# Performance work log

Hardware: AMD Instinct MI355X
Metric: run time of the kernel (lower is better)

Reference implementation:

```python
import jax, jax.numpy as jnp
import numpy as np

B, C, M, T = 2, 512, 16, 128
H = 8
D = C // H  # 64, divisible by 4 for 2D RoPE
G = C // 4  # GroupNorm groups = 128
S = M * T


def group_norm(x, scale, bias, groups=G, eps=1e-5):
    b, c, m, t = x.shape
    xg = x.reshape(b, groups, c // groups, m, t)
    mu = xg.mean(axis=(2, 3, 4), keepdims=True)
    var = xg.var(axis=(2, 3, 4), keepdims=True)
    xn = ((xg - mu) * jax.lax.rsqrt(var + eps)).reshape(b, c, m, t)
    return xn * scale[None, :, None, None] + bias[None, :, None, None]


def dwsep_conv(x, dw, pw):
    # depthwise 3x3 (groups=C) then pointwise 1x1
    y = jax.lax.conv_general_dilated(
        x, dw, window_strides=(1, 1), padding='SAME',
        dimension_numbers=('NCHW', 'HWIO', 'NCHW'), feature_group_count=x.shape[1])
    return jnp.einsum('bcmt,cd->bdmt', y, pw)


def rope2d(x):
    # x: [B,H,M,T,D]; first D/2 dims rotated by freq index m, last D/2 by time index t
    d = x.shape[-1]
    dh = d // 2
    q = dh // 2
    inv = 1.0 / (10000.0 ** (jnp.arange(q, dtype=jnp.float32) / q))

    def rot(v, ang):
        h = v.shape[-1] // 2
        v1, v2 = v[..., :h], v[..., h:]
        c, s = jnp.cos(ang), jnp.sin(ang)
        return jnp.concatenate([v1 * c - v2 * s, v1 * s + v2 * c], axis=-1)

    ang_f = jnp.arange(x.shape[2], dtype=jnp.float32)[:, None] * inv  # [M,q]
    ang_t = jnp.arange(x.shape[3], dtype=jnp.float32)[:, None] * inv  # [T,q]
    xf = rot(x[..., :dh], ang_f[:, None, :])  # broadcast over T
    xt = rot(x[..., dh:], ang_t)
    return jnp.concatenate([xf, xt], axis=-1)


def setup_inputs() -> dict:
    key = jax.random.key(0)
    ks = jax.random.split(key, 14)
    s = 0.02
    return {
        'x': jax.random.normal(ks[0], (B, C, M, T), jnp.float32),
        'lengths': jax.random.randint(ks[1], (B,), T // 2, T + 1),
        'gn_scale': jnp.ones((C,), jnp.float32),
        'gn_bias': jnp.zeros((C,), jnp.float32),
        'dw_q': jax.random.normal(ks[2], (3, 3, 1, C), jnp.float32) * s,
        'dw_k': jax.random.normal(ks[3], (3, 3, 1, C), jnp.float32) * s,
        'dw_v': jax.random.normal(ks[4], (3, 3, 1, C), jnp.float32) * s,
        'pw_q': jax.random.normal(ks[5], (C, C), jnp.float32) * s,
        'pw_k': jax.random.normal(ks[6], (C, C), jnp.float32) * s,
        'pw_v': jax.random.normal(ks[7], (C, C), jnp.float32) * s,
        'attn_w': jax.random.normal(ks[8], (C, C), jnp.float32) * s,
        'attn_b': jnp.zeros((C,), jnp.float32),
        'out_w': jax.random.normal(ks[9], (C, C), jnp.float32) * s,
        'out_b': jnp.zeros((C,), jnp.float32),
    }


def reference(x, lengths, gn_scale, gn_bias, dw_q, dw_k, dw_v, pw_q, pw_k, pw_v,
              attn_w, attn_b, out_w, out_b):
    residual = x
    xn = group_norm(x, gn_scale, gn_bias)

    def to_heads(y):  # [B,C,M,T] -> [B,H,M,T,D]
        return y.reshape(B, H, D, M, T).transpose(0, 1, 3, 4, 2)

    q = rope2d(to_heads(dwsep_conv(xn, dw_q, pw_q)))
    k = rope2d(to_heads(dwsep_conv(xn, dw_k, pw_k)))
    v = to_heads(dwsep_conv(xn, dw_v, pw_v))

    q = q.reshape(B, H, S, D)
    k = k.reshape(B, H, S, D)
    v = v.reshape(B, H, S, D)

    scores = jnp.einsum('bhsd,bhkd->bhsk', q, k) / np.sqrt(D).astype(np.float32)
    valid_t = jnp.arange(T)[None, :] < lengths[:, None]        # [B,T]
    valid = jnp.tile(valid_t, (1, M))                          # [B,S], token idx = m*T + t
    scores = jnp.where(valid[:, None, None, :], scores, jnp.float32(-1e9))
    attn = jax.nn.softmax(scores, axis=-1)
    o = jnp.einsum('bhsk,bhkd->bhsd', attn, v)                 # [B,H,S,D]

    o = o.transpose(0, 2, 1, 3).reshape(B, S, C)
    o = o @ attn_w + attn_b                                    # block output proj
    o = o.reshape(B, M, T, C).transpose(0, 3, 1, 2)            # [B,C,M,T]
    out = jnp.einsum('bcmt,cd->bdmt', o, out_w) + out_b[None, :, None, None]
    return residual + out
```

## Files before the change

kernel.cpp:

```cpp
#include <hip/hip_runtime.h>
#include <math.h>

#define CCH 512
#define SSQ 2048
#define MTOT 4096

typedef __bf16 bf16;
typedef __bf16 bf16x8 __attribute__((ext_vector_type(8)));
typedef __bf16 bf16x4 __attribute__((ext_vector_type(4)));
typedef float  f32x4  __attribute__((ext_vector_type(4)));

#define AS1 __attribute__((address_space(1)))
#define AS3 __attribute__((address_space(3)))
__device__ __forceinline__ void glds16(const void* g, void* l) {
    __builtin_amdgcn_global_load_lds((const AS1 void*)g, (AS3 void*)l, 16, 0, 0);
}

__global__ __launch_bounds__(256) void gnw_kernel(const float* __restrict__ x,
        float* __restrict__ mu, float* __restrict__ rstd,
        const float* __restrict__ w0, const float* __restrict__ w1,
        const float* __restrict__ w2, const float* __restrict__ w3,
        const float* __restrict__ w4, bf16* __restrict__ wT) {
    __shared__ float smem[64*65];
    int tid = threadIdx.x;
    if (blockIdx.x < 256) {
        float* s_sum = smem;
        float* s_sq  = smem + 256;
        int bg = blockIdx.x;
        long base = (long)bg * 8192;
        float sum = 0.f, sq = 0.f;
#pragma unroll
        for (int r = 0; r < 32; ++r) {
            float v = x[base + r*256 + tid];
            sum += v; sq += v*v;
        }
        s_sum[tid] = sum; s_sq[tid] = sq;
        __syncthreads();
        for (int off = 128; off > 0; off >>= 1) {
            if (tid < off) { s_sum[tid] += s_sum[tid+off]; s_sq[tid] += s_sq[tid+off]; }
            __syncthreads();
        }
        if (tid == 0) {
            float m = s_sum[0] * (1.f/8192.f);
            float v = s_sq[0]  * (1.f/8192.f) - m*m;
            mu[bg] = m;
            rstd[bg] = rsqrtf(v + 1e-5f);
        }
    } else {
        int bid = blockIdx.x - 256;
        int z = bid >> 6, r2 = bid & 63;
        int k0 = (r2 >> 3)*64, n0 = (r2 & 7)*64;
        const float* srcs[5] = {w0, w1, w2, w3, w4};
        const float* W = srcs[z];
        bf16* D = wT + (long)z * (CCH*CCH);
        float (*t)[65] = (float(*)[65])smem;
        int cI = tid & 63, r4 = tid >> 6;
#pragma unroll
        for (int p = 0; p < 16; ++p) {
            int kr = p*4 + r4;
            t[kr][cI] = W[(long)(k0+kr)*CCH + n0 + cI];
        }
        __syncthreads();
#pragma unroll
        for (int p = 0; p < 16; ++p) {
            int nr = p*4 + r4;
            D[(long)(n0+nr)*CCH + k0 + cI] = (bf16)t[cI][nr];
        }
    }
}

__global__ void tn_kernel(const float* __restrict__ x, const float* __restrict__ mu,
                          const float* __restrict__ rstd, const float* __restrict__ gsc,
                          const float* __restrict__ gbs, bf16* __restrict__ xnT) {
    __shared__ float t[64][65];
    int s0 = blockIdx.x*64, c0 = blockIdx.y*64, b = blockIdx.z;
    int tid = threadIdx.x;
    int cI = tid & 63, r4 = tid >> 6;
#pragma unroll
    for (int p = 0; p < 16; ++p) {
        int cr = p*4 + r4;
        t[cr][cI] = x[((long)(b*CCH + c0 + cr))*SSQ + s0 + cI];
    }
    __syncthreads();
#pragma unroll
    for (int p = 0; p < 16; ++p) {
        int sr = p*4 + r4;
        int c = c0 + cI;
        int g = b*128 + (c >> 2);
        float v = (t[cI][sr] - mu[g]) * rstd[g] * gsc[c] + gbs[c];
        xnT[((long)(b*SSQ + s0 + sr))*CCH + c] = (bf16)v;
    }
}

__global__ __launch_bounds__(256) void dw3_kernel(const bf16* __restrict__ xnT,
        const float* __restrict__ dwq, const float* __restrict__ dwk,
        const float* __restrict__ dwv,
        bf16* __restrict__ yq, bf16* __restrict__ yk, bf16* __restrict__ yv) {
    int tid = threadIdx.x;
    int cc = (tid & 63) * 8;
    int s  = blockIdx.x*4 + (tid >> 6);
    int sl = s & (SSQ-1);
    int b  = s >> 11;
    int m = sl >> 7, t = sl & 127;
    float aq[8] = {}, ak[8] = {}, av[8] = {};
#pragma unroll
    for (int di = 0; di < 3; ++di) {
        int m2 = m + di - 1;
        if ((unsigned)m2 >= 16u) continue;
#pragma unroll
        for (int dj = 0; dj < 3; ++dj) {
            int t2 = t + dj - 1;
            if ((unsigned)t2 >= 128u) continue;
            bf16x8 xv = *(const bf16x8*)(xnT + ((long)(b*SSQ + m2*128 + t2))*CCH + cc);
            int wi = (di*3 + dj)*CCH + cc;
#pragma unroll
            for (int i = 0; i < 8; ++i) {
                float xf = (float)xv[i];
                aq[i] += xf * dwq[wi+i];
                ak[i] += xf * dwk[wi+i];
                av[i] += xf * dwv[wi+i];
            }
        }
    }
    bf16x8 oq, ok, ov;
#pragma unroll
    for (int i = 0; i < 8; ++i) { oq[i] = (bf16)aq[i]; ok[i] = (bf16)ak[i]; ov[i] = (bf16)av[i]; }
    long o = (long)s*CCH + cc;
    *(bf16x8*)(yq + o) = oq;
    *(bf16x8*)(yk + o) = ok;
    *(bf16x8*)(yv + o) = ov;
}

template<int NFR>
__device__ __forceinline__ void gemm_core128(const bf16* __restrict__ A,
        const bf16* __restrict__ Wt, int m0, int n0,
        bf16* As, bf16* Bs, f32x4 (&acc)[4][NFR]) {
    int tid = threadIdx.x, lane = tid & 63, wid = tid >> 6;
    int sw = wid & 1, nw = wid >> 1;
    int col = lane & 15, quad = lane >> 4;
    const char* gA[4]; char* ldsA[4];
#pragma unroll
    for (int p = 0; p < 4; ++p) {
        int ci = tid + p*256;
        int row = ci >> 3;
        int c = (ci & 7) ^ (row & 7);
        gA[p] = (const char*)A + ((long)(m0+row)*CCH + c*8)*2;
        ldsA[p] = (char*)As + ci*16;
    }
    const char* gB[NFR]; char* ldsB[NFR];
#pragma unroll
    for (int p = 0; p < NFR; ++p) {
        int ci = tid + p*256;
        int row = ci >> 3;
        int c = (ci & 7) ^ (row & 7);
        gB[p] = (const char*)Wt + ((long)(n0+row)*CCH + c*8)*2;
        ldsB[p] = (char*)Bs + ci*16;
    }
    int rowA = sw*64 + col;
    int rowB = nw*(NFR*16) + col;
    for (int k0 = 0; k0 < CCH; k0 += 64) {
        __syncthreads();
#pragma unroll
        for (int p = 0; p < 4; ++p)   glds16(gA[p] + k0*2, ldsA[p]);
#pragma unroll
        for (int p = 0; p < NFR; ++p) glds16(gB[p] + k0*2, ldsB[p]);
        __syncthreads();
        bf16x8 af[4][2], bfr[NFR][2];
#pragma unroll
        for (int mt = 0; mt < 4; ++mt) {
            int r = rowA + mt*16;
#pragma unroll
            for (int ks = 0; ks < 2; ++ks) {
                int c = (ks*4 + quad) ^ (r & 7);
                af[mt][ks] = *(const bf16x8*)((char*)As + r*128 + c*16);
            }
        }
#pragma unroll
        for (int nt = 0; nt < NFR; ++nt) {
            int r = rowB + nt*16;
#pragma unroll
            for (int ks = 0; ks < 2; ++ks) {
                int c = (ks*4 + quad) ^ (r & 7);
                bfr[nt][ks] = *(const bf16x8*)((char*)Bs + r*128 + c*16);
            }
        }
#pragma unroll
        for (int ks = 0; ks < 2; ++ks)
#pragma unroll
            for (int mt = 0; mt < 4; ++mt)
#pragma unroll
                for (int nt = 0; nt < NFR; ++nt)
                    acc[mt][nt] = __builtin_amdgcn_mfma_f32_16x16x32_bf16(
                        af[mt][ks], bfr[nt][ks], acc[mt][nt], 0,0,0);
    }
}

__global__ __launch_bounds__(256) void gemm_qkv(const bf16* __restrict__ Abase,
        const bf16* __restrict__ wT, bf16* __restrict__ qout,
        bf16* __restrict__ kout, bf16* __restrict__ vout) {
    __shared__ bf16 As[128*64];
    __shared__ bf16 Bs[64*64];
    int m0 = blockIdx.x*128, n0 = blockIdx.y*64, z = blockIdx.z;
    f32x4 acc[4][2] = {};
    gemm_core128<2>(Abase + (long)z*MTOT*CCH, wT + (long)z*CCH*CCH, m0, n0, As, Bs, acc);
    int tid = threadIdx.x, lane = tid & 63, wid = tid >> 6;
    int sw = wid & 1, nw = wid >> 1;
    int col = lane & 15, quad = lane >> 4;
    int nb = n0 + nw*32, mb = m0 + sw*64;
    if (z < 2) {
        bf16* outp = z ? kout : qout;
        const float sc = z ? 1.0f : 0.125f;
        float invf = __expf(-(float)col * 0.5756462732485114f);
        bool tHalf = (nb & 32) != 0;
#pragma unroll
        for (int mt = 0; mt < 4; ++mt)
#pragma unroll
            for (int r = 0; r < 4; ++r) {
                int row = mb + mt*16 + quad*4 + r;
                int sl = row & (SSQ-1);
                float pos = tHalf ? (float)(sl & 127) : (float)(sl >> 7);
                float ang = pos * invf;
                float sn, cs;
                __sincosf(ang, &sn, &cs);
                float x1 = acc[mt][0][r], x2 = acc[mt][1][r];
                outp[(long)row*CCH + nb + col]      = (bf16)((x1*cs - x2*sn)*sc);
                outp[(long)row*CCH + nb + 16 + col] = (bf16)((x1*sn + x2*cs)*sc);
            }
    } else {
#pragma unroll
        for (int mt = 0; mt < 4; ++mt)
#pragma unroll
            for (int nt = 0; nt < 2; ++nt) {
                int n = nb + nt*16 + col;
                int row0 = mb + mt*16 + quad*4;
                int bq = row0 >> 11, sl0 = row0 & (SSQ-1);
                bf16x4 pk;
#pragma unroll
                for (int r = 0; r < 4; ++r) pk[r] = (bf16)acc[mt][nt][r];
                *(bf16x4*)(vout + ((long)(bq*CCH + n))*SSQ + sl0) = pk;
            }
    }
}

template<int MODE>
__global__ __launch_bounds__(256) void gemm_bf16(const bf16* __restrict__ A,
        const bf16* __restrict__ Wt, const float* __restrict__ bias,
        const float* __restrict__ resid, void* __restrict__ outv) {
    __shared__ bf16 As[128*64];
    __shared__ bf16 Bs[64*64];
    int m0 = blockIdx.x*128, n0 = blockIdx.y*64;
    f32x4 acc[4][2] = {};
    gemm_core128<2>(A, Wt, m0, n0, As, Bs, acc);
    int tid = threadIdx.x, lane = tid & 63, wid = tid >> 6;
    int sw = wid & 1, nw = wid >> 1;
    int col = lane & 15, quad = lane >> 4;
    int nb = n0 + nw*32, mb = m0 + sw*64;
    if (MODE == 3) {
        bf16* outp = (bf16*)outv;
#pragma unroll
        for (int nt = 0; nt < 2; ++nt) {
            int n = nb + nt*16 + col;
            float bv = bias[n];
#pragma unroll
            for (int mt = 0; mt < 4; ++mt)
#pragma unroll
                for (int r = 0; r < 4; ++r)
                    outp[(long)(mb + mt*16 + quad*4 + r)*CCH + n] = (bf16)(acc[mt][nt][r] + bv);
        }
    } else {
        float* outp = (float*)outv;
#pragma unroll
        for (int mt = 0; mt < 4; ++mt)
#pragma unroll
            for (int nt = 0; nt < 2; ++nt) {
                int n = nb + nt*16 + col;
                float bv = bias[n];
                int row0 = mb + mt*16 + quad*4;
                int b = row0 >> 11, sl0 = row0 & (SSQ-1);
                long off = ((long)(b*CCH + n))*SSQ + sl0;
                float4 rr = *(const float4*)(resid + off);
                float4 o4;
                o4.x = acc[mt][nt][0] + bv + rr.x;
                o4.y = acc[mt][nt][1] + bv + rr.y;
                o4.z = acc[mt][nt][2] + bv + rr.z;
                o4.w = acc[mt][nt][3] + bv + rr.w;
                *(float4*)(outp + off) = o4;
            }
    }
}

__global__ __launch_bounds__(256) void attn_kernel(
        const bf16* __restrict__ qb, const bf16* __restrict__ kb,
        const bf16* __restrict__ vb, const int* __restrict__ lengths,
        float* __restrict__ opart, float* __restrict__ lpart) {
    __shared__ char KV[2][16384];
    __shared__ bf16 Ps[4][32*72];
    int bid = blockIdx.x;
    int bh = bid & 15;
    int n  = bid >> 4;
    int qt = n & 15, kvh = n >> 4;
    int b = bh >> 3, h = bh & 7;
    int tid = threadIdx.x, wid = tid >> 6, lane = tid & 63;
    int col = lane & 15, quad = lane >> 4;
    int lenb = lengths[b];
    int q0 = qt*128 + wid*32;
    int k0 = kvh*1024;

    const char* gp[4]; long gstep[4]; int ldsoff[4];
#pragma unroll
    for (int p = 0; p < 4; ++p) {
        int idx = tid + p*256;
        int isV = idx >> 9;
        int rem = idx & 511;
        int r = rem >> 3;
        int csrc = (rem & 7) ^ (r & 7);
        if (!isV) { gp[p] = (const char*)kb + ((long)(b*SSQ + k0 + r))*1024 + h*128 + csrc*16; gstep[p] = 65536; }
        else      { gp[p] = (const char*)vb + ((long)(b*CCH + h*64 + r))*4096 + (long)k0*2 + csrc*16; gstep[p] = 128; }
        ldsoff[p] = idx*16;
    }

    f32x4 mb[4];
#pragma unroll
    for (int sub = 0; sub < 4; ++sub)
#pragma unroll
        for (int r = 0; r < 4; ++r)
            mb[sub][r] = (64 + sub*16 + quad*4 + r < lenb) ? 0.f : -10000.f;

    const bf16* qp = qb + (long)(b*SSQ)*CCH + h*64;
    bf16x8 qf[2][2];
#pragma unroll
    for (int qt2 = 0; qt2 < 2; ++qt2)
#pragma unroll
        for (int dc = 0; dc < 2; ++dc)
            qf[qt2][dc] = *(const bf16x8*)(qp + (long)(q0 + qt2*16 + col)*CCH + dc*32 + quad*8);

    f32x4 of[2][4] = {};
    float ls0 = 0.f, ls1 = 0.f;
    bf16* pw = Ps[wid];
    int cswz = col & 7;

#pragma unroll
    for (int p = 0; p < 4; ++p) glds16(gp[p], KV[0] + ldsoff[p]);
    __syncthreads();

    for (int t = 0; t < 16; ++t) {
        if (t < 15) {
#pragma unroll
            for (int p = 0; p < 4; ++p)
                glds16(gp[p] + (long)(t+1)*gstep[p], KV[(t+1) & 1] + ldsoff[p]);
        }
        const bf16* K = (const bf16*)(KV[t & 1]);
        const bf16* V = (const bf16*)(KV[t & 1] + 8192);
        bool masked = ((kvh*16 + t) & 1) != 0;
        f32x4 sc[4][2];
#pragma unroll
        for (int sub = 0; sub < 4; ++sub)
#pragma unroll
            for (int qt2 = 0; qt2 < 2; ++qt2)
                sc[sub][qt2] = masked ? mb[sub] : (f32x4){0.f,0.f,0.f,0.f};
#pragma unroll
        for (int sub = 0; sub < 4; ++sub)
#pragma unroll
            for (int dc = 0; dc < 2; ++dc) {
                bf16x8 kf = *(const bf16x8*)((const char*)K + (sub*16 + col)*128 + (((dc*4+quad) ^ cswz))*16);
#pragma unroll
                for (int qt2 = 0; qt2 < 2; ++qt2)
                    sc[sub][qt2] = __builtin_amdgcn_mfma_f32_16x16x32_bf16(
                        kf, qf[qt2][dc], sc[sub][qt2], 0,0,0);
            }
#pragma unroll
        for (int sub = 0; sub < 4; ++sub)
#pragma unroll
            for (int qt2 = 0; qt2 < 2; ++qt2) {
                bf16x4 pk;
#pragma unroll
                for (int r = 0; r < 4; ++r) {
                    float p = __expf(sc[sub][qt2][r]);
                    if (qt2) ls1 += p; else ls0 += p;
                    pk[r] = (bf16)p;
                }
                *(bf16x4*)(pw + (qt2*16 + col)*72 + sub*16 + quad*4) = pk;
            }
#pragma unroll
        for (int ks = 0; ks < 2; ++ks) {
            bf16x8 pf0 = *(const bf16x8*)(pw + col*72 + ks*32 + quad*8);
            bf16x8 pf1 = *(const bf16x8*)(pw + (16 + col)*72 + ks*32 + quad*8);
#pragma unroll
            for (int dt = 0; dt < 4; ++dt) {
                bf16x8 vf = *(const bf16x8*)((const char*)V + (dt*16 + col)*128 + (((ks*4+quad) ^ cswz))*16);
                of[0][dt] = __builtin_amdgcn_mfma_f32_16x16x32_bf16(pf0, vf, of[0][dt], 0,0,0);
                of[1][dt] = __builtin_amdgcn_mfma_f32_16x16x32_bf16(pf1, vf, of[1][dt], 0,0,0);
            }
        }
        __syncthreads();
    }

    ls0 += __shfl_xor(ls0, 16); ls0 += __shfl_xor(ls0, 32);
    ls1 += __shfl_xor(ls1, 16); ls1 += __shfl_xor(ls1, 32);

    float* op = opart + ((long)(kvh*16 + bh)*2048)*64;
#pragma unroll
    for (int qt2 = 0; qt2 < 2; ++qt2)
#pragma unroll
        for (int dt = 0; dt < 4; ++dt)
#pragma unroll
            for (int r = 0; r < 4; ++r)
                op[(long)(q0 + qt2*16 + quad*4 + r)*64 + dt*16 + col] = of[qt2][dt][r];
    if (quad == 0) {
        float* lp = lpart + (long)(kvh*16 + bh)*2048;
        lp[q0 + col]      = ls0;
        lp[q0 + 16 + col] = ls1;
    }
}

__global__ __launch_bounds__(256) void attn_merge(const float* __restrict__ opart,
        const float* __restrict__ lpart, bf16* __restrict__ o) {
    int idx = blockIdx.x*256 + threadIdx.x;
    int dchunk = idx & 15;
    int q = (idx >> 4) & 2047;
    int bh = idx >> 15;
    long o0 = ((long)bh*2048 + q)*64 + dchunk*4;
    float4 a = *(const float4*)(opart + o0);
    float4 c = *(const float4*)(opart + o0 + (long)16*2048*64);
    float inv = 1.f / (lpart[bh*2048 + q] + lpart[(16 + bh)*2048 + q]);
    bf16x4 pk;
    pk[0] = (bf16)((a.x + c.x) * inv);
    pk[1] = (bf16)((a.y + c.y) * inv);
    pk[2] = (bf16)((a.z + c.z) * inv);
    pk[3] = (bf16)((a.w + c.w) * inv);
    int b = bh >> 3, h = bh & 7;
    *(bf16x4*)(o + ((long)(b*SSQ + q))*CCH + h*64 + dchunk*4) = pk;
}

extern "C" void kernel_launch(void* const* d_in, const int* in_sizes, int n_in,
                              void* d_out, int out_size, void* d_ws, size_t ws_size,
                              hipStream_t stream) {
    const float* x        = (const float*)d_in[0];
    const int*   lengths  = (const int*)  d_in[1];
    const float* gn_scale = (const float*)d_in[2];
    const float* gn_bias  = (const float*)d_in[3];
    const float* dw_q     = (const float*)d_in[4];
    const float* dw_k     = (const float*)d_in[5];
    const float* dw_v     = (const float*)d_in[6];
    const float* pw_q     = (const float*)d_in[7];
    const float* pw_k     = (const float*)d_in[8];
    const float* pw_v     = (const float*)d_in[9];
    const float* attn_w   = (const float*)d_in[10];
    const float* attn_b   = (const float*)d_in[11];
    const float* out_w    = (const float*)d_in[12];
    const float* out_b    = (const float*)d_in[13];
    float* out = (float*)d_out;

    char* w = (char*)d_ws;
    float* mu   = (float*)w;
    float* rstd = (float*)(w + 1024);
    bf16* wT    = (bf16*)(w + 4096);
    bf16* wTa = wT + 3*CCH*CCH;
    bf16* wTo = wT + 4*CCH*CCH;
    float* lpart = (float*)(w + 0x00290000);
    bf16* xnT  = (bf16*)(w + 0x00300000);
    bf16* yT   = (bf16*)(w + 0x00700000);
    float* opart = (float*)(w + 0x00300000);
    bf16* qbf  = (bf16*)(w + 0x01300000);
    bf16* kbf  = (bf16*)(w + 0x01700000);
    bf16* vbf  = (bf16*)(w + 0x01B00000);
    bf16* obf  = (bf16*)(w + 0x01F00000);
    bf16* tmpb = (bf16*)(w + 0x02300000);

    gnw_kernel<<<576, 256, 0, stream>>>(x, mu, rstd, pw_q, pw_k, pw_v, attn_w, out_w, wT);
    tn_kernel<<<dim3(32,8,2), 256, 0, stream>>>(x, mu, rstd, gn_scale, gn_bias, xnT);
    dw3_kernel<<<MTOT/4, 256, 0, stream>>>(xnT, dw_q, dw_k, dw_v,
                                           yT, yT + (long)MTOT*CCH, yT + (long)2*MTOT*CCH);

    gemm_qkv<<<dim3(MTOT/128, CCH/64, 3), 256, 0, stream>>>(yT, wT, qbf, kbf, vbf);

    attn_kernel<<<512, 256, 0, stream>>>(qbf, kbf, vbf, lengths, opart, lpart);
    attn_merge<<<2048, 256, 0, stream>>>(opart, lpart, obf);

    dim3 gg(MTOT/128, CCH/64);
    gemm_bf16<3><<<gg, 256, 0, stream>>>(obf, wTa, attn_b, nullptr, tmpb);
    gemm_bf16<4><<<gg, 256, 0, stream>>>(tmpb, wTo, out_b, x, out);
}
```

Measured before the change: 170.5 us.

## Fold attn/out projections into one GEMM and merge split-KV attention in-block

Measured after the change: 168.1 us. About the same (-1.4%).

```diff
diff --git a/kernel.cpp b/kernel.cpp
--- a/kernel.cpp
+++ b/kernel.cpp
@@ -20,7 +20,9 @@
         float* __restrict__ mu, float* __restrict__ rstd,
         const float* __restrict__ w0, const float* __restrict__ w1,
         const float* __restrict__ w2, const float* __restrict__ w3,
-        const float* __restrict__ w4, bf16* __restrict__ wT) {
+        const float* __restrict__ w4, bf16* __restrict__ wT,
+        const float* __restrict__ attnb, const float* __restrict__ outb,
+        float* __restrict__ bcv) {
     __shared__ float smem[64*65];
     int tid = threadIdx.x;
     if (blockIdx.x < 256) {
@@ -46,7 +48,7 @@
             mu[bg] = m;
             rstd[bg] = rsqrtf(v + 1e-5f);
         }
-    } else {
+    } else if (blockIdx.x < 576) {
         int bid = blockIdx.x - 256;
         int z = bid >> 6, r2 = bid & 63;
         int k0 = (r2 >> 3)*64, n0 = (r2 & 7)*64;
@@ -66,6 +68,18 @@
             int nr = p*4 + r4;
             D[(long)(n0+nr)*CCH + k0 + cI] = (bf16)t[cI][nr];
         }
+    } else if (blockIdx.x < 578) {
+        int n = (blockIdx.x - 576)*256 + tid;
+        float a = outb[n];
+        for (int j = 0; j < 512; ++j)
+            a = fmaf(attnb[j], w4[(long)j*CCH + n], a);
+        bcv[n] = a;
+    } else {
+        bf16* wAc = wT + (long)5*CCH*CCH;
+        int base = (blockIdx.x - 578)*4096 + tid;
+#pragma unroll
+        for (int p = 0; p < 16; ++p)
+            wAc[base + p*256] = (bf16)w3[base + p*256];
     }
 }
 
@@ -196,18 +210,33 @@
 }
 
 __global__ __launch_bounds__(256) void gemm_qkv(const bf16* __restrict__ Abase,
-        const bf16* __restrict__ wT, bf16* __restrict__ qout,
+        bf16* __restrict__ wT, bf16* __restrict__ qout,
         bf16* __restrict__ kout, bf16* __restrict__ vout) {
     __shared__ bf16 As[128*64];
     __shared__ bf16 Bs[64*64];
-    int m0 = blockIdx.x*128, n0 = blockIdx.y*64, z = blockIdx.z;
+    int z = blockIdx.z;
+    if (z == 3 && blockIdx.x >= 4) return;
+    int m0 = blockIdx.x*128, n0 = blockIdx.y*64;
+    const bf16* Aop = (z < 3) ? Abase + (long)z*MTOT*CCH : wT + (long)4*CCH*CCH;
+    const bf16* Wop = (z < 3) ? wT + (long)z*CCH*CCH   : wT + (long)5*CCH*CCH;
     f32x4 acc[4][2] = {};
-    gemm_core128<2>(Abase + (long)z*MTOT*CCH, wT + (long)z*CCH*CCH, m0, n0, As, Bs, acc);
+    gemm_core128<2>(Aop, Wop, m0, n0, As, Bs, acc);
     int tid = threadIdx.x, lane = tid & 63, wid = tid >> 6;
     int sw = wid & 1, nw = wid >> 1;
     int col = lane & 15, quad = lane >> 4;
     int nb = n0 + nw*32, mb = m0 + sw*64;
-    if (z < 2) {
+    if (z == 3) {
+        bf16* wCt = wT + (long)6*CCH*CCH;
+#pragma unroll
+        for (int nt = 0; nt < 2; ++nt) {
+            int n = nb + nt*16 + col;
+#pragma unroll
+            for (int mt = 0; mt < 4; ++mt)
+#pragma unroll
+                for (int r = 0; r < 4; ++r)
+                    wCt[(long)(mb + mt*16 + quad*4 + r)*CCH + n] = (bf16)acc[mt][nt][r];
+        }
+    } else if (z < 2) {
         bf16* outp = z ? kout : qout;
         const float sc = z ? 1.0f : 0.125f;
         float invf = __expf(-(float)col * 0.5756462732485114f);
@@ -242,10 +271,9 @@
     }
 }
 
-template<int MODE>
-__global__ __launch_bounds__(256) void gemm_bf16(const bf16* __restrict__ A,
+__global__ __launch_bounds__(256) void gemm_out(const bf16* __restrict__ A,
         const bf16* __restrict__ Wt, const float* __restrict__ bias,
-        const float* __restrict__ resid, void* __restrict__ outv) {
+        const float* __restrict__ resid, float* __restrict__ outp) {
     __shared__ bf16 As[128*64];
     __shared__ bf16 Bs[64*64];
     int m0 = blockIdx.x*128, n0 = blockIdx.y*64;
@@ -255,67 +283,53 @@
     int sw = wid & 1, nw = wid >> 1;
     int col = lane & 15, quad = lane >> 4;
     int nb = n0 + nw*32, mb = m0 + sw*64;
-    if (MODE == 3) {
-        bf16* outp = (bf16*)outv;
+#pragma unroll
+    for (int mt = 0; mt < 4; ++mt)
 #pragma unroll
         for (int nt = 0; nt < 2; ++nt) {
             int n = nb + nt*16 + col;
             float bv = bias[n];
-#pragma unroll
-            for (int mt = 0; mt < 4; ++mt)
-#pragma unroll
-                for (int r = 0; r < 4; ++r)
-                    outp[(long)(mb + mt*16 + quad*4 + r)*CCH + n] = (bf16)(acc[mt][nt][r] + bv);
-        }
-    } else {
-        float* outp = (float*)outv;
-#pragma unroll
-        for (int mt = 0; mt < 4; ++mt)
-#pragma unroll
-            for (int nt = 0; nt < 2; ++nt) {
-                int n = nb + nt*16 + col;
-                float bv = bias[n];
-                int row0 = mb + mt*16 + quad*4;
-                int b = row0 >> 11, sl0 = row0 & (SSQ-1);
-                long off = ((long)(b*CCH + n))*SSQ + sl0;
-                float4 rr = *(const float4*)(resid + off);
-                float4 o4;
-                o4.x = acc[mt][nt][0] + bv + rr.x;
-                o4.y = acc[mt][nt][1] + bv + rr.y;
-                o4.z = acc[mt][nt][2] + bv + rr.z;
-                o4.w = acc[mt][nt][3] + bv + rr.w;
-                *(float4*)(outp + off) = o4;
-            }
-    }
-}
-
-__global__ __launch_bounds__(256) void attn_kernel(
+            int row0 = mb + mt*16 + quad*4;
+            int b = row0 >> 11, sl0 = row0 & (SSQ-1);
+            long off = ((long)(b*CCH + n))*SSQ + sl0;
+            float4 rr = *(const float4*)(resid + off);
+            float4 o4;
+            o4.x = acc[mt][nt][0] + bv + rr.x;
+            o4.y = acc[mt][nt][1] + bv + rr.y;
+            o4.z = acc[mt][nt][2] + bv + rr.z;
+            o4.w = acc[mt][nt][3] + bv + rr.w;
+            *(float4*)(outp + off) = o4;
+        }
+}
+
+__global__ __launch_bounds__(512) void attn_kernel(
         const bf16* __restrict__ qb, const bf16* __restrict__ kb,
         const bf16* __restrict__ vb, const int* __restrict__ lengths,
-        float* __restrict__ opart, float* __restrict__ lpart) {
-    __shared__ char KV[2][16384];
-    __shared__ bf16 Ps[4][32*72];
+        bf16* __restrict__ o) {
+    __shared__ char KVs[2][32768];
+    __shared__ bf16 Ps[8][32*72];
+    __shared__ float Lm[4][2][16];
     int bid = blockIdx.x;
-    int bh = bid & 15;
-    int n  = bid >> 4;
-    int qt = n & 15, kvh = n >> 4;
+    int bh = bid & 15, qtb = bid >> 4;
     int b = bh >> 3, h = bh & 7;
     int tid = threadIdx.x, wid = tid >> 6, lane = tid & 63;
     int col = lane & 15, quad = lane >> 4;
+    int qh = wid & 3, kh = wid >> 2;
+    int q0 = qtb*128 + qh*32;
     int lenb = lengths[b];
-    int q0 = qt*128 + wid*32;
-    int k0 = kvh*1024;
 
     const char* gp[4]; long gstep[4]; int ldsoff[4];
 #pragma unroll
     for (int p = 0; p < 4; ++p) {
-        int idx = tid + p*256;
-        int isV = idx >> 9;
-        int rem = idx & 511;
+        int idx = tid + p*512;
+        int half = idx >> 10;
+        int rem2 = idx & 1023;
+        int isV = rem2 >> 9;
+        int rem = rem2 & 511;
         int r = rem >> 3;
         int csrc = (rem & 7) ^ (r & 7);
-        if (!isV) { gp[p] = (const char*)kb + ((long)(b*SSQ + k0 + r))*1024 + h*128 + csrc*16; gstep[p] = 65536; }
-        else      { gp[p] = (const char*)vb + ((long)(b*CCH + h*64 + r))*4096 + (long)k0*2 + csrc*16; gstep[p] = 128; }
+        if (!isV) { gp[p] = (const char*)kb + ((long)(b*SSQ + half*1024 + r))*1024 + h*128 + csrc*16; gstep[p] = 65536; }
+        else      { gp[p] = (const char*)vb + ((long)(b*CCH + h*64 + r))*4096 + half*2048 + csrc*16;  gstep[p] = 128; }
         ldsoff[p] = idx*16;
     }
 
@@ -340,18 +354,18 @@
     int cswz = col & 7;
 
 #pragma unroll
-    for (int p = 0; p < 4; ++p) glds16(gp[p], KV[0] + ldsoff[p]);
+    for (int p = 0; p < 4; ++p) glds16(gp[p], KVs[0] + ldsoff[p]);
     __syncthreads();
 
     for (int t = 0; t < 16; ++t) {
         if (t < 15) {
 #pragma unroll
             for (int p = 0; p < 4; ++p)
-                glds16(gp[p] + (long)(t+1)*gstep[p], KV[(t+1) & 1] + ldsoff[p]);
-        }
-        const bf16* K = (const bf16*)(KV[t & 1]);
-        const bf16* V = (const bf16*)(KV[t & 1] + 8192);
-        bool masked = ((kvh*16 + t) & 1) != 0;
+                glds16(gp[p] + (long)(t+1)*gstep[p], KVs[(t+1) & 1] + ldsoff[p]);
+        }
+        const bf16* K = (const bf16*)(KVs[t & 1] + kh*16384);
+        const bf16* V = (const bf16*)(KVs[t & 1] + kh*16384 + 8192);
+        bool masked = (t & 1) != 0;
         f32x4 sc[4][2];
 #pragma unroll
         for (int sub = 0; sub < 4; ++sub)
@@ -398,38 +412,37 @@
     ls0 += __shfl_xor(ls0, 16); ls0 += __shfl_xor(ls0, 32);
     ls1 += __shfl_xor(ls1, 16); ls1 += __shfl_xor(ls1, 32);
 
-    float* op = opart + ((long)(kvh*16 + bh)*2048)*64;
-#pragma unroll
-    for (int qt2 = 0; qt2 < 2; ++qt2)
-#pragma unroll
-        for (int dt = 0; dt < 4; ++dt)
-#pragma unroll
-            for (int r = 0; r < 4; ++r)
-                op[(long)(q0 + qt2*16 + quad*4 + r)*64 + dt*16 + col] = of[qt2][dt][r];
-    if (quad == 0) {
-        float* lp = lpart + (long)(kvh*16 + bh)*2048;
-        lp[q0 + col]      = ls0;
-        lp[q0 + 16 + col] = ls1;
-    }
-}
-
-__global__ __launch_bounds__(256) void attn_merge(const float* __restrict__ opart,
-        const float* __restrict__ lpart, bf16* __restrict__ o) {
-    int idx = blockIdx.x*256 + threadIdx.x;
-    int dchunk = idx & 15;
-    int q = (idx >> 4) & 2047;
-    int bh = idx >> 15;
-    long o0 = ((long)bh*2048 + q)*64 + dchunk*4;
-    float4 a = *(const float4*)(opart + o0);
-    float4 c = *(const float4*)(opart + o0 + (long)16*2048*64);
-    float inv = 1.f / (lpart[bh*2048 + q] + lpart[(16 + bh)*2048 + q]);
-    bf16x4 pk;
-    pk[0] = (bf16)((a.x + c.x) * inv);
-    pk[1] = (bf16)((a.y + c.y) * inv);
-    pk[2] = (bf16)((a.z + c.z) * inv);
-    pk[3] = (bf16)((a.w + c.w) * inv);
-    int b = bh >> 3, h = bh & 7;
-    *(bf16x4*)(o + ((long)(b*SSQ + q))*CCH + h*64 + dchunk*4) = pk;
+    float* Om = (float*)KVs;
+    if (kh == 1) {
+#pragma unroll
+        for (int qt2 = 0; qt2 < 2; ++qt2)
+#pragma unroll
+            for (int dt = 0; dt < 4; ++dt)
+#pragma unroll
+                for (int r = 0; r < 4; ++r)
+                    Om[(qh*32 + qt2*16 + quad*4 + r)*64 + dt*16 + col] = of[qt2][dt][r];
+        if (quad == 0) { Lm[qh][0][col] = ls0; Lm[qh][1][col] = ls1; }
+    }
+    __syncthreads();
+    if (kh == 0) {
+        float i0 = 1.f / (ls0 + Lm[qh][0][col]);
+        float i1 = 1.f / (ls1 + Lm[qh][1][col]);
+        bf16* ob = o + (long)(b*SSQ + q0)*CCH + h*64;
+#pragma unroll
+        for (int qt2 = 0; qt2 < 2; ++qt2) {
+            float inv = qt2 ? i1 : i0;
+            float ir[4];
+#pragma unroll
+            for (int r = 0; r < 4; ++r) ir[r] = __shfl(inv, quad*4 + r);
+#pragma unroll
+            for (int dt = 0; dt < 4; ++dt)
+#pragma unroll
+                for (int r = 0; r < 4; ++r) {
+                    float v = of[qt2][dt][r] + Om[(qh*32 + qt2*16 + quad*4 + r)*64 + dt*16 + col];
+                    ob[(long)(qt2*16 + quad*4 + r)*CCH + dt*16 + col] = (bf16)(v * ir[r]);
+                }
+        }
+    }
 }
 
 extern "C" void kernel_launch(void* const* d_in, const int* in_sizes, int n_in,
@@ -454,30 +467,25 @@
     char* w = (char*)d_ws;
     float* mu   = (float*)w;
     float* rstd = (float*)(w + 1024);
+    float* bcv  = (float*)(w + 2048);
     bf16* wT    = (bf16*)(w + 4096);
-    bf16* wTa = wT + 3*CCH*CCH;
-    bf16* wTo = wT + 4*CCH*CCH;
-    float* lpart = (float*)(w + 0x00290000);
-    bf16* xnT  = (bf16*)(w + 0x00300000);
-    bf16* yT   = (bf16*)(w + 0x00700000);
-    float* opart = (float*)(w + 0x00300000);
-    bf16* qbf  = (bf16*)(w + 0x01300000);
-    bf16* kbf  = (bf16*)(w + 0x01700000);
-    bf16* vbf  = (bf16*)(w + 0x01B00000);
-    bf16* obf  = (bf16*)(w + 0x01F00000);
-    bf16* tmpb = (bf16*)(w + 0x02300000);
-
-    gnw_kernel<<<576, 256, 0, stream>>>(x, mu, rstd, pw_q, pw_k, pw_v, attn_w, out_w, wT);
+    bf16* wCt = wT + (long)6*CCH*CCH;
+    bf16* xnT  = (bf16*)(w + 0x00400000);
+    bf16* yT   = (bf16*)(w + 0x00800000);
+    bf16* qbf  = (bf16*)(w + 0x01400000);
+    bf16* kbf  = (bf16*)(w + 0x01800000);
+    bf16* vbf  = (bf16*)(w + 0x01C00000);
+    bf16* obf  = (bf16*)(w + 0x02000000);
+
+    gnw_kernel<<<642, 256, 0, stream>>>(x, mu, rstd, pw_q, pw_k, pw_v, attn_w, out_w,
+                                        wT, attn_b, out_b, bcv);
     tn_kernel<<<dim3(32,8,2), 256, 0, stream>>>(x, mu, rstd, gn_scale, gn_bias, xnT);
     dw3_kernel<<<MTOT/4, 256, 0, stream>>>(xnT, dw_q, dw_k, dw_v,
                                            yT, yT + (long)MTOT*CCH, yT + (long)2*MTOT*CCH);
 
-    gemm_qkv<<<dim3(MTOT/128, CCH/64, 3), 256, 0, stream>>>(yT, wT, qbf, kbf, vbf);
-
-    attn_kernel<<<512, 256, 0, stream>>>(qbf, kbf, vbf, lengths, opart, lpart);
-    attn_merge<<<2048, 256, 0, stream>>>(opart, lpart, obf);
-
-    dim3 gg(MTOT/128, CCH/64);
-    gemm_bf16<3><<<gg, 256, 0, stream>>>(obf, wTa, attn_b, nullptr, tmpb);
-    gemm_bf16<4><<<gg, 256, 0, stream>>>(tmpb, wTo, out_b, x, out);
-}
+    gemm_qkv<<<dim3(MTOT/128, CCH/64, 4), 256, 0, stream>>>(yT, wT, qbf, kbf, vbf);
+
+    attn_kernel<<<256, 512, 0, stream>>>(qbf, kbf, vbf, lengths, obf);
+
+    gemm_out<<<dim3(MTOT/128, CCH/64), 256, 0, stream>>>(obf, wCt, bcv, x, out);
+}
```
